# Kernel tuning notes

Hardware: AMD Instinct MI355X
Metric: run time of the kernel (lower is better)

Reference implementation:

```python
import jax, jax.numpy as jnp
import numpy as np

B, L, IN_DIM, D_MODEL, N_LAYERS = 4, 1024, 64, 512, 3
D_INNER, STATE, DT_RANK, K = 1024, 16, 32, 4  # expand=2, dt_rank=d_model//16, conv kernel 4


def setup_inputs() -> dict:
    key = jax.random.key(0)
    ks = jax.random.split(key, 8)
    s = 0.02
    def rn(k, shp):
        return jax.random.normal(k, shp, jnp.float32) * s
    inp = {"x": jax.random.normal(ks[0], (B, L, IN_DIM), jnp.float32)}
    inp["input_w"] = rn(ks[1], (D_MODEL, IN_DIM)); inp["input_b"] = jnp.zeros((D_MODEL,), jnp.float32)
    inp["in_proj_w"] = rn(ks[2], (N_LAYERS, 2 * D_INNER, D_MODEL)); inp["in_proj_b"] = jnp.zeros((N_LAYERS, 2 * D_INNER), jnp.float32)
    inp["conv_w"] = rn(ks[3], (N_LAYERS, D_INNER, 1, K)); inp["conv_b"] = jnp.zeros((N_LAYERS, D_INNER), jnp.float32)
    inp["x_proj_w"] = rn(ks[4], (N_LAYERS, DT_RANK + 2 * STATE, D_INNER))
    inp["dt_proj_w"] = rn(ks[5], (N_LAYERS, D_INNER, DT_RANK)); inp["dt_proj_b"] = jnp.full((N_LAYERS, D_INNER), -4.0, jnp.float32)
    inp["A_log"] = jnp.tile(jnp.log(jnp.arange(1, STATE + 1, dtype=jnp.float32))[None, None, :], (N_LAYERS, D_INNER, 1))
    inp["D"] = jnp.ones((N_LAYERS, D_INNER), jnp.float32)
    inp["out_proj_w"] = rn(ks[6], (N_LAYERS, D_MODEL, D_INNER)); inp["out_proj_b"] = jnp.zeros((N_LAYERS, D_MODEL), jnp.float32)
    inp["ln_w"] = jnp.ones((N_LAYERS, D_MODEL), jnp.float32); inp["ln_b"] = jnp.zeros((N_LAYERS, D_MODEL), jnp.float32)
    return inp


def _layernorm(x, w, b):
    mu = jnp.mean(x, -1, keepdims=True)
    v = jnp.var(x, -1, keepdims=True)
    return (x - mu) * jax.lax.rsqrt(v + 1e-5) * w + b


def _mamba(u, iw, ib, cw, cb, xw, dw, db, A_log, Dp, ow, ob):
    # u: [B, L, d_model]
    xz = u @ iw.T + ib                          # [B, L, 2*d_inner]
    xp, z = jnp.split(xz, 2, axis=-1)
    # causal depthwise conv over time
    xc = jax.lax.conv_general_dilated(xp.transpose(0, 2, 1), cw, (1,), [(K - 1, 0)],
                                      feature_group_count=D_INNER,
                                      dimension_numbers=("NCH", "OIH", "NCH")) + cb[None, :, None]
    xc = jax.nn.silu(xc).transpose(0, 2, 1)     # [B, L, d_inner]
    proj = xc @ xw.T                            # [B, L, dt_rank + 2*N]
    dtl = proj[..., :DT_RANK]
    Bm = proj[..., DT_RANK:DT_RANK + STATE]
    Cm = proj[..., DT_RANK + STATE:]
    dt = jax.nn.softplus(dtl @ dw.T + db)       # [B, L, d_inner]
    A = -jnp.exp(A_log)                         # [d_inner, N]

    def step(h, t):
        dt_t, B_t, C_t, x_t = t                 # [B,d], [B,N], [B,N], [B,d]
        h = h * jnp.exp(dt_t[..., None] * A) + (dt_t * x_t)[..., None] * B_t[:, None, :]
        return h, jnp.einsum("bdn,bn->bd", h, C_t)

    h0 = jnp.zeros((u.shape[0], D_INNER, STATE), u.dtype)
    _, ys = jax.lax.scan(step, h0, (dt.transpose(1, 0, 2), Bm.transpose(1, 0, 2),
                                    Cm.transpose(1, 0, 2), xc.transpose(1, 0, 2)))
    y = ys.transpose(1, 0, 2) + xc * Dp
    y = y * jax.nn.silu(z)
    return y @ ow.T + ob


def reference(x, input_w, input_b, in_proj_w, in_proj_b, conv_w, conv_b, x_proj_w,
              dt_proj_w, dt_proj_b, A_log, D, out_proj_w, out_proj_b, ln_w, ln_b):
    h = x @ input_w.T + input_b                 # [B, L, d_model]
    for i in range(N_LAYERS):
        res = h
        h = _mamba(h, in_proj_w[i], in_proj_b[i], conv_w[i], conv_b[i], x_proj_w[i],
                   dt_proj_w[i], dt_proj_b[i], A_log[i], D[i], out_proj_w[i], out_proj_b[i])
        h = _layernorm(h + res, ln_w[i], ln_b[i])
    return h[:, -1, :]
```

## Files before the change

kernel.cpp:

```cpp
#include <hip/hip_runtime.h>
#include <hip/hip_bf16.h>
#include <cstddef>
#include <cstdint>

#define NB 4
#define NL 1024
#define IN_DIM 64
#define D_MODEL 512
#define N_LAYERS 3
#define D_INNER 1024
#define NSTATE 16
#define DT_RANK 32
#define KCONV 4
#define NROWS (NB * NL)
#define CHUNK 16
#define NCHUNK (NL / CHUNK)
#define LOG2E 1.4426950408889634f

typedef __attribute__((ext_vector_type(8))) short short8;
typedef __attribute__((ext_vector_type(4))) float f32x4;
typedef __attribute__((ext_vector_type(4))) unsigned short us4;
typedef unsigned short ushort_t;

__device__ __forceinline__ ushort_t f2b1(float x) {
  uint32_t u = __builtin_bit_cast(uint32_t, x);
  u += 0x7fffu + ((u >> 16) & 1u);
  return (ushort_t)(u >> 16);
}
__device__ __forceinline__ float b2f(ushort_t u) {
  return __builtin_bit_cast(float, (uint32_t)u << 16);
}

__device__ __forceinline__ void gload_lds16(const ushort_t* src, short* dst) {
  __builtin_amdgcn_global_load_lds(
      (const __attribute__((address_space(1))) uint32_t*)src,
      (__attribute__((address_space(3))) uint32_t*)dst, 16, 0, 0);
}

#define E0 (NROWS * IN_DIM)
#define E1 (D_MODEL * IN_DIM)
#define E2 (N_LAYERS * 2 * D_INNER * D_MODEL)
#define E3 (N_LAYERS * 64 * D_INNER)
#define E4 (N_LAYERS * D_INNER * DT_RANK)
#define E5 (N_LAYERS * D_MODEL * D_INNER)
#define ETOT (E0 + E1 + E2 + E3 + E4 + E5)

__global__ __launch_bounds__(256) void cvt_all(
    const float* __restrict__ x, const float* __restrict__ inw,
    const float* __restrict__ ipw, const float* __restrict__ xpw,
    const float* __restrict__ dpw, const float* __restrict__ opw,
    ushort_t* __restrict__ xb, ushort_t* __restrict__ inwb,
    ushort_t* __restrict__ iwb, ushort_t* __restrict__ xwb,
    ushort_t* __restrict__ dwb, ushort_t* __restrict__ owb)
{
  int i = (blockIdx.x * 256 + threadIdx.x) * 4;
  if (i >= ETOT) return;
  const float* src; ushort_t* dst; int off;
  if      (i < E0)                  { src = x;   dst = xb;   off = i; }
  else if (i < E0+E1)               { src = inw; dst = inwb; off = i - E0; }
  else if (i < E0+E1+E2)            { src = ipw; dst = iwb;  off = i - (E0+E1); }
  else if (i < E0+E1+E2+E3)         { src = xpw; dst = xwb;  off = i - (E0+E1+E2); }
  else if (i < E0+E1+E2+E3+E4)      { src = dpw; dst = dwb;  off = i - (E0+E1+E2+E3); }
  else                              { src = opw; dst = owb;  off = i - (E0+E1+E2+E3+E4); }
  const float4 v = *(const float4*)(src + off);
  us4 o;
  o.x = f2b1(v.x); o.y = f2b1(v.y); o.z = f2b1(v.z); o.w = f2b1(v.w);
  *(us4*)(dst + off) = o;
}

template<int BM, int BN, int MF, int NF, int ACT, bool WF32, bool WB16>
__global__ __launch_bounds__(256) void gemm_mfma(
    const ushort_t* __restrict__ A, int lda,
    const ushort_t* __restrict__ W,
    const float* __restrict__ bias,
    float* __restrict__ Cf, ushort_t* __restrict__ Cb,
    int M, int N, int K)
{
  constexpr int CA = BM / 64;
  constexpr int CB = BN / 64;
  __shared__ __align__(16) short sa[BM * 32];
  __shared__ __align__(16) short sb[BN * 32];

  const int tid = threadIdx.x;
  const int l = tid & 63;
  const int wid = tid >> 6;
  const int wrow = (wid >> 1) * (BM / 2);
  const int wcol = (wid & 1) * (BN / 2);
  const int m0 = blockIdx.y * BM;
  const int n0 = blockIdx.x * BN;

  const int srow = l >> 2;
  const int scol = (l & 3) * 8;

  f32x4 acc[MF][NF] = {};

  for (int k0 = 0; k0 < K; k0 += 32) {
#pragma unroll
    for (int c = 0; c < CA; ++c) {
      short* dst = sa + (c * 4 + wid) * 512;
      const ushort_t* src =
          A + (size_t)(m0 + (c * 4 + wid) * 16 + srow) * lda + k0 + scol;
      gload_lds16(src, dst);
    }
#pragma unroll
    for (int c = 0; c < CB; ++c) {
      short* dst = sb + (c * 4 + wid) * 512;
      const ushort_t* src =
          W + (size_t)(n0 + (c * 4 + wid) * 16 + srow) * K + k0 + scol;
      gload_lds16(src, dst);
    }
    __syncthreads();

    short8 af[MF], bfr[NF];
#pragma unroll
    for (int mi = 0; mi < MF; ++mi)
      af[mi] = *(const short8*)(sa + (wrow + mi * 16 + (l & 15)) * 32 + (l >> 4) * 8);
#pragma unroll
    for (int nj = 0; nj < NF; ++nj)
      bfr[nj] = *(const short8*)(sb + (wcol + nj * 16 + (l & 15)) * 32 + (l >> 4) * 8);
#pragma unroll
    for (int mi = 0; mi < MF; ++mi)
#pragma unroll
      for (int nj = 0; nj < NF; ++nj)
        acc[mi][nj] = __builtin_amdgcn_mfma_f32_16x16x32_bf16(
            af[mi], bfr[nj], acc[mi][nj], 0, 0, 0);
    __syncthreads();
  }

#pragma unroll
  for (int nj = 0; nj < NF; ++nj) {
    const int col = n0 + wcol + nj * 16 + (l & 15);
    const float bv = bias ? bias[col] : 0.f;
#pragma unroll
    for (int mi = 0; mi < MF; ++mi) {
#pragma unroll
      for (int q = 0; q < 4; ++q) {
        const int row = m0 + wrow + mi * 16 + (l >> 4) * 4 + q;
        float v = acc[mi][nj][q] + bv;
        if (ACT == 1) v = (v > 20.f) ? v : log1pf(__expf(v));
        if (WF32) Cf[(size_t)row * N + col] = v;
        if (WB16) Cb[(size_t)row * N + col] = f2b1(v);
      }
    }
  }
}

__global__ __launch_bounds__(256) void conv_silu(
    const ushort_t* __restrict__ xzb,
    const float* __restrict__ cw,
    const float* __restrict__ cb,
    ushort_t* __restrict__ xcb)
{
  const int idx = blockIdx.x * 256 + threadIdx.x;
  const int d4 = (idx & (D_INNER / 4 - 1)) * 4;
  const int bt = idx >> 8;
  const int t = bt & (NL - 1);
  const int b = bt >> 10;

  float acc4[4];
  {
    const float4 cbv = *(const float4*)(cb + d4);
    acc4[0] = cbv.x; acc4[1] = cbv.y; acc4[2] = cbv.z; acc4[3] = cbv.w;
  }
  float wv[4][4];
#pragma unroll
  for (int i = 0; i < 4; ++i) {
    const float4 w = *(const float4*)(cw + (size_t)(d4 + i) * KCONV);
    wv[i][0] = w.x; wv[i][1] = w.y; wv[i][2] = w.z; wv[i][3] = w.w;
  }
#pragma unroll
  for (int j = 0; j < KCONV; ++j) {
    const int tt = t - (KCONV - 1) + j;
    if (tt >= 0) {
      const us4 xv = *(const us4*)(xzb + (size_t)(b * NL + tt) * (2 * D_INNER) + d4);
      acc4[0] = fmaf(b2f(xv.x), wv[0][j], acc4[0]);
      acc4[1] = fmaf(b2f(xv.y), wv[1][j], acc4[1]);
      acc4[2] = fmaf(b2f(xv.z), wv[2][j], acc4[2]);
      acc4[3] = fmaf(b2f(xv.w), wv[3][j], acc4[3]);
    }
  }
  us4 o;
#pragma unroll
  for (int i = 0; i < 4; ++i) {
    const float s = acc4[i] / (1.f + __expf(-acc4[i]));
    ((ushort_t*)&o)[i] = f2b1(s);
  }
  *(us4*)(xcb + (size_t)idx * 4) = o;
}

__global__ __launch_bounds__(256) void scan_fused(
    const ushort_t* __restrict__ dtb,
    const float* __restrict__ proj,
    const ushort_t* __restrict__ xcb,
    const ushort_t* __restrict__ xzb,
    const float* __restrict__ A_log,
    const float* __restrict__ Dp,
    ushort_t* __restrict__ yb)
{
  __shared__ float S_lds[NCHUNK][4][NSTATE + 1];
  __shared__ float H_lds[NCHUNK][4][NSTATE + 1];
  __shared__ float sdt_lds[NCHUNK][4];

  const int tid = threadIdx.x;
  const int c = tid >> 2;
  const int dl = tid & 3;
  const int d = blockIdx.x * 4 + dl;
  const int b = blockIdx.y;

  float A2[NSTATE];
#pragma unroll
  for (int n = 0; n < NSTATE; ++n)
    A2[n] = -__expf(A_log[d * NSTATE + n]) * LOG2E;

  const int t0 = c * CHUNK;
  float h[NSTATE];
#pragma unroll
  for (int n = 0; n < NSTATE; ++n) h[n] = 0.f;
  float sdt = 0.f;

  for (int tt = 0; tt < CHUNK; ++tt) {
    const size_t row = (size_t)(b * NL + t0 + tt);
    const float dtv = b2f(dtb[row * D_INNER + d]);
    const float xv = b2f(xcb[row * D_INNER + d]);
    const float* pr = proj + row * 64;
    float Bv[NSTATE];
    *(float4*)(Bv)      = *(const float4*)(pr + 32);
    *(float4*)(Bv + 4)  = *(const float4*)(pr + 36);
    *(float4*)(Bv + 8)  = *(const float4*)(pr + 40);
    *(float4*)(Bv + 12) = *(const float4*)(pr + 44);
    sdt += dtv;
    const float dx = dtv * xv;
#pragma unroll
    for (int n = 0; n < NSTATE; ++n)
      h[n] = fmaf(h[n], exp2f(dtv * A2[n]), dx * Bv[n]);
  }
  sdt_lds[c][dl] = sdt;
#pragma unroll
  for (int n = 0; n < NSTATE; ++n) S_lds[c][dl][n] = h[n];
  __syncthreads();

  if (tid < 64) {
    const int dl2 = tid >> 4;
    const int n2 = tid & 15;
    const float A2n = -__expf(A_log[(blockIdx.x * 4 + dl2) * NSTATE + n2]) * LOG2E;
    float H = 0.f;
    for (int cc = 0; cc < NCHUNK; ++cc) {
      H_lds[cc][dl2][n2] = H;
      H = fmaf(H, exp2f(A2n * sdt_lds[cc][dl2]), S_lds[cc][dl2][n2]);
    }
  }
  __syncthreads();

#pragma unroll
  for (int n = 0; n < NSTATE; ++n) h[n] = H_lds[c][dl][n];
  const float Dv = Dp[d];

  for (int tt = 0; tt < CHUNK; ++tt) {
    const size_t row = (size_t)(b * NL + t0 + tt);
    const size_t rd = row * D_INNER + d;
    const float dtv = b2f(dtb[rd]);
    const float xv = b2f(xcb[rd]);
    const float* pr = proj + row * 64;
    float Bv[NSTATE], Cv[NSTATE];
    *(float4*)(Bv)      = *(const float4*)(pr + 32);
    *(float4*)(Bv + 4)  = *(const float4*)(pr + 36);
    *(float4*)(Bv + 8)  = *(const float4*)(pr + 40);
    *(float4*)(Bv + 12) = *(const float4*)(pr + 44);
    *(float4*)(Cv)      = *(const float4*)(pr + 48);
    *(float4*)(Cv + 4)  = *(const float4*)(pr + 52);
    *(float4*)(Cv + 8)  = *(const float4*)(pr + 56);
    *(float4*)(Cv + 12) = *(const float4*)(pr + 60);
    const float dx = dtv * xv;
    float accv = 0.f;
#pragma unroll
    for (int n = 0; n < NSTATE; ++n) {
      h[n] = fmaf(h[n], exp2f(dtv * A2[n]), dx * Bv[n]);
      accv = fmaf(h[n], Cv[n], accv);
    }
    const float zv = b2f(xzb[row * (2 * D_INNER) + D_INNER + d]);
    float yv = fmaf(xv, Dv, accv);
    yv *= zv / (1.f + __expf(-zv));
    yb[rd] = f2b1(yv);
  }
}

__global__ __launch_bounds__(256) void add_ln(
    const float* __restrict__ x,
    const float* __restrict__ res,
    const float* __restrict__ w,
    const float* __restrict__ bln,
    float* __restrict__ out,
    ushort_t* __restrict__ outb,
    float* __restrict__ out2)
{
  const int wave = threadIdx.x >> 6;
  const int lane = threadIdx.x & 63;
  const int row = blockIdx.x * 4 + wave;
  const float* xr = x + (size_t)row * D_MODEL;
  const float* rr = res + (size_t)row * D_MODEL;

  float v[8];
  float s = 0.f, s2 = 0.f;
#pragma unroll
  for (int i = 0; i < 8; ++i) {
    const float t = xr[lane + i * 64] + rr[lane + i * 64];
    v[i] = t; s += t; s2 = fmaf(t, t, s2);
  }
#pragma unroll
  for (int off = 32; off; off >>= 1) {
    s += __shfl_xor(s, off);
    s2 += __shfl_xor(s2, off);
  }
  const float mean = s * (1.f / D_MODEL);
  const float var = s2 * (1.f / D_MODEL) - mean * mean;
  const float rstd = rsqrtf(var + 1e-5f);
  const bool last_t = (row & (NL - 1)) == (NL - 1);
#pragma unroll
  for (int i = 0; i < 8; ++i) {
    const int c = lane + i * 64;
    const float o = (v[i] - mean) * rstd * w[c] + bln[c];
    out[(size_t)row * D_MODEL + c] = o;
    outb[(size_t)row * D_MODEL + c] = f2b1(o);
    if (out2 && last_t) out2[(size_t)(row >> 10) * D_MODEL + c] = o;
  }
}

extern "C" void kernel_launch(void* const* d_in, const int* in_sizes, int n_in,
                              void* d_out, int out_size, void* d_ws, size_t ws_size,
                              hipStream_t stream)
{
  const float* x         = (const float*)d_in[0];
  const float* input_w   = (const float*)d_in[1];
  const float* input_b   = (const float*)d_in[2];
  const float* in_proj_w = (const float*)d_in[3];
  const float* in_proj_b = (const float*)d_in[4];
  const float* conv_w    = (const float*)d_in[5];
  const float* conv_b    = (const float*)d_in[6];
  const float* x_proj_w  = (const float*)d_in[7];
  const float* dt_proj_w = (const float*)d_in[8];
  const float* dt_proj_b = (const float*)d_in[9];
  const float* A_log     = (const float*)d_in[10];
  const float* Dp        = (const float*)d_in[11];
  const float* out_proj_w= (const float*)d_in[12];
  const float* out_proj_b= (const float*)d_in[13];
  const float* ln_w      = (const float*)d_in[14];
  const float* ln_b      = (const float*)d_in[15];

  float* p = (float*)d_ws;
  float* h0   = p; p += (size_t)NROWS * D_MODEL;
  float* h1   = p; p += (size_t)NROWS * D_MODEL;
  float* tmp  = p; p += (size_t)NROWS * D_MODEL;
  float* proj = p; p += (size_t)NROWS * 64;
  ushort_t* q = (ushort_t*)p;
  ushort_t* xzb   = q; q += (size_t)NROWS * 2 * D_INNER;
  ushort_t* xcb   = q; q += (size_t)NROWS * D_INNER;
  ushort_t* dtbb  = q; q += (size_t)NROWS * D_INNER;
  ushort_t* projb = q; q += (size_t)NROWS * 64;
  ushort_t* yb    = q; q += (size_t)NROWS * D_INNER;
  ushort_t* hb    = q; q += (size_t)NROWS * D_MODEL;
  ushort_t* xb    = q; q += (size_t)E0;
  ushort_t* inwb  = q; q += (size_t)E1;
  ushort_t* iwb   = q; q += (size_t)E2;
  ushort_t* xwb   = q; q += (size_t)E3;
  ushort_t* dwb   = q; q += (size_t)E4;
  ushort_t* owb   = q; q += (size_t)E5;

  cvt_all<<<(ETOT / 4 + 255) / 256, 256, 0, stream>>>(
      x, input_w, in_proj_w, x_proj_w, dt_proj_w, out_proj_w,
      xb, inwb, iwb, xwb, dwb, owb);

  gemm_mfma<64, 64, 2, 2, 0, true, true>
      <<<dim3(D_MODEL / 64, NROWS / 64), 256, 0, stream>>>(
      xb, IN_DIM, inwb, input_b, h0, hb, NROWS, D_MODEL, IN_DIM);

  float* hc = h0;
  float* hn = h1;

  for (int l = 0; l < N_LAYERS; ++l) {
    const ushort_t* iw = iwb + (size_t)l * 2 * D_INNER * D_MODEL;
    const float* ib = in_proj_b + (size_t)l * 2 * D_INNER;
    const float* cw = conv_w    + (size_t)l * D_INNER * KCONV;
    const float* cb = conv_b    + (size_t)l * D_INNER;
    const ushort_t* xw = xwb + (size_t)l * 64 * D_INNER;
    const ushort_t* dw = dwb + (size_t)l * D_INNER * DT_RANK;
    const float* db = dt_proj_b + (size_t)l * D_INNER;
    const float* Al = A_log     + (size_t)l * D_INNER * NSTATE;
    const float* Dl = Dp        + (size_t)l * D_INNER;
    const ushort_t* ow = owb + (size_t)l * D_MODEL * D_INNER;
    const float* ob = out_proj_b+ (size_t)l * D_MODEL;
    const float* lw = ln_w      + (size_t)l * D_MODEL;
    const float* lb = ln_b      + (size_t)l * D_MODEL;

    gemm_mfma<128, 128, 4, 4, 0, false, true>
        <<<dim3(2 * D_INNER / 128, NROWS / 128), 256, 0, stream>>>(
        hb, D_MODEL, iw, ib, nullptr, xzb, NROWS, 2 * D_INNER, D_MODEL);

    conv_silu<<<NROWS * D_INNER / 4 / 256, 256, 0, stream>>>(xzb, cw, cb, xcb);

    gemm_mfma<64, 64, 2, 2, 0, true, true>
        <<<dim3(1, NROWS / 64), 256, 0, stream>>>(
        xcb, D_INNER, xw, nullptr, proj, projb, NROWS, 64, D_INNER);

    gemm_mfma<128, 128, 4, 4, 1, false, true>
        <<<dim3(D_INNER / 128, NROWS / 128), 256, 0, stream>>>(
        projb, 64, dw, db, nullptr, dtbb, NROWS, D_INNER, DT_RANK);

    scan_fused<<<dim3(D_INNER / 4, NB), 256, 0, stream>>>(
        dtbb, proj, xcb, xzb, Al, Dl, yb);

    gemm_mfma<64, 64, 2, 2, 0, true, false>
        <<<dim3(D_MODEL / 64, NROWS / 64), 256, 0, stream>>>(
        yb, D_INNER, ow, ob, tmp, nullptr, NROWS, D_MODEL, D_INNER);

    add_ln<<<NROWS / 4, 256, 0, stream>>>(
        tmp, hc, lw, lb, hn, hb,
        (l == N_LAYERS - 1) ? (float*)d_out : nullptr);

    float* t2 = hc; hc = hn; hn = t2;
  }
}
```

Measured before the change: 634.8 us.

## Split fused chunked scan into three kernels with coalesced d-major thread mapping

Replaces the single fused chunked-scan kernel, which mapped 4 channels by 64 chunks per block and did the carry through LDS, with three kernels. Phase 1 computes per-chunk local states, a separate carry kernel propagates chunk states across time, and phase 2 recomputes the outputs. Threads now map to consecutive channels, so loads of dt and x are coalesced. The cost is extra global round-trips for the chunk states and two more launches. The out_proj GEMM tile also grows from 64x64 to 128x128, which launches fewer, larger blocks.

```diff
diff --git a/kernel.cpp b/kernel.cpp
--- a/kernel.cpp
+++ b/kernel.cpp
@@ -188,36 +188,30 @@
   *(us4*)(xcb + (size_t)idx * 4) = o;
 }
 
-__global__ __launch_bounds__(256) void scan_fused(
+__global__ __launch_bounds__(256) void scan_phase1(
     const ushort_t* __restrict__ dtb,
     const float* __restrict__ proj,
     const ushort_t* __restrict__ xcb,
-    const ushort_t* __restrict__ xzb,
     const float* __restrict__ A_log,
-    const float* __restrict__ Dp,
-    ushort_t* __restrict__ yb)
-{
-  __shared__ float S_lds[NCHUNK][4][NSTATE + 1];
-  __shared__ float H_lds[NCHUNK][4][NSTATE + 1];
-  __shared__ float sdt_lds[NCHUNK][4];
-
-  const int tid = threadIdx.x;
-  const int c = tid >> 2;
-  const int dl = tid & 3;
-  const int d = blockIdx.x * 4 + dl;
-  const int b = blockIdx.y;
+    float* __restrict__ S_loc,
+    float* __restrict__ sumdt)
+{
+  const int d = blockIdx.x * 256 + threadIdx.x;
+  const int c = blockIdx.y;
+  const int b = blockIdx.z;
 
   float A2[NSTATE];
 #pragma unroll
   for (int n = 0; n < NSTATE; ++n)
     A2[n] = -__expf(A_log[d * NSTATE + n]) * LOG2E;
 
-  const int t0 = c * CHUNK;
   float h[NSTATE];
 #pragma unroll
   for (int n = 0; n < NSTATE; ++n) h[n] = 0.f;
   float sdt = 0.f;
 
+  const int t0 = c * CHUNK;
+#pragma unroll 4
   for (int tt = 0; tt < CHUNK; ++tt) {
     const size_t row = (size_t)(b * NL + t0 + tt);
     const float dtv = b2f(dtb[row * D_INNER + d]);
@@ -234,27 +228,65 @@
     for (int n = 0; n < NSTATE; ++n)
       h[n] = fmaf(h[n], exp2f(dtv * A2[n]), dx * Bv[n]);
   }
-  sdt_lds[c][dl] = sdt;
-#pragma unroll
-  for (int n = 0; n < NSTATE; ++n) S_lds[c][dl][n] = h[n];
-  __syncthreads();
-
-  if (tid < 64) {
-    const int dl2 = tid >> 4;
-    const int n2 = tid & 15;
-    const float A2n = -__expf(A_log[(blockIdx.x * 4 + dl2) * NSTATE + n2]) * LOG2E;
-    float H = 0.f;
-    for (int cc = 0; cc < NCHUNK; ++cc) {
-      H_lds[cc][dl2][n2] = H;
-      H = fmaf(H, exp2f(A2n * sdt_lds[cc][dl2]), S_lds[cc][dl2][n2]);
-    }
-  }
-  __syncthreads();
-
-#pragma unroll
-  for (int n = 0; n < NSTATE; ++n) h[n] = H_lds[c][dl][n];
+
+  const size_t cbase = (size_t)(b * NCHUNK + c);
+  sumdt[cbase * D_INNER + d] = sdt;
+#pragma unroll
+  for (int n = 0; n < NSTATE; ++n)
+    S_loc[(cbase * NSTATE + n) * D_INNER + d] = h[n];
+}
+
+__global__ __launch_bounds__(256) void scan_carry(
+    const float* __restrict__ S_loc,
+    const float* __restrict__ sumdt,
+    const float* __restrict__ A_log,
+    float* __restrict__ H_in)
+{
+  const int idx = blockIdx.x * 256 + threadIdx.x;
+  const int d = idx & (D_INNER - 1);
+  const int n = (idx >> 10) & (NSTATE - 1);
+  const int b = idx >> 14;
+
+  const float A2n = -__expf(A_log[d * NSTATE + n]) * LOG2E;
+
+  float H = 0.f;
+  for (int c = 0; c < NCHUNK; ++c) {
+    const size_t cbase = (size_t)(b * NCHUNK + c);
+    H_in[(cbase * NSTATE + n) * D_INNER + d] = H;
+    const float sdt = sumdt[cbase * D_INNER + d];
+    H = fmaf(H, exp2f(A2n * sdt), S_loc[(cbase * NSTATE + n) * D_INNER + d]);
+  }
+}
+
+__global__ __launch_bounds__(256) void scan_phase2(
+    const ushort_t* __restrict__ dtb,
+    const float* __restrict__ proj,
+    const ushort_t* __restrict__ xcb,
+    const ushort_t* __restrict__ xzb,
+    const float* __restrict__ A_log,
+    const float* __restrict__ Dp,
+    const float* __restrict__ H_in,
+    ushort_t* __restrict__ yb)
+{
+  const int d = blockIdx.x * 256 + threadIdx.x;
+  const int c = blockIdx.y;
+  const int b = blockIdx.z;
+
+  float A2[NSTATE];
+#pragma unroll
+  for (int n = 0; n < NSTATE; ++n)
+    A2[n] = -__expf(A_log[d * NSTATE + n]) * LOG2E;
+
+  const size_t cbase = (size_t)(b * NCHUNK + c);
+  float h[NSTATE];
+#pragma unroll
+  for (int n = 0; n < NSTATE; ++n)
+    h[n] = H_in[(cbase * NSTATE + n) * D_INNER + d];
+
   const float Dv = Dp[d];
-
+  const int t0 = c * CHUNK;
+
+#pragma unroll 4
   for (int tt = 0; tt < CHUNK; ++tt) {
     const size_t row = (size_t)(b * NL + t0 + tt);
     const size_t rd = row * D_INNER + d;
@@ -351,6 +383,9 @@
   float* h1   = p; p += (size_t)NROWS * D_MODEL;
   float* tmp  = p; p += (size_t)NROWS * D_MODEL;
   float* proj = p; p += (size_t)NROWS * 64;
+  float* Sloc = p; p += (size_t)NB * NCHUNK * NSTATE * D_INNER;
+  float* Hin  = p; p += (size_t)NB * NCHUNK * NSTATE * D_INNER;
+  float* sdt  = p; p += (size_t)NB * NCHUNK * D_INNER;
   ushort_t* q = (ushort_t*)p;
   ushort_t* xzb   = q; q += (size_t)NROWS * 2 * D_INNER;
   ushort_t* xcb   = q; q += (size_t)NROWS * D_INNER;
@@ -405,11 +440,15 @@
         <<<dim3(D_INNER / 128, NROWS / 128), 256, 0, stream>>>(
         projb, 64, dw, db, nullptr, dtbb, NROWS, D_INNER, DT_RANK);
 
-    scan_fused<<<dim3(D_INNER / 4, NB), 256, 0, stream>>>(
-        dtbb, proj, xcb, xzb, Al, Dl, yb);
-
-    gemm_mfma<64, 64, 2, 2, 0, true, false>
-        <<<dim3(D_MODEL / 64, NROWS / 64), 256, 0, stream>>>(
+    scan_phase1<<<dim3(D_INNER / 256, NCHUNK, NB), 256, 0, stream>>>(
+        dtbb, proj, xcb, Al, Sloc, sdt);
+    scan_carry<<<(NB * NSTATE * D_INNER) / 256, 256, 0, stream>>>(
+        Sloc, sdt, Al, Hin);
+    scan_phase2<<<dim3(D_INNER / 256, NCHUNK, NB), 256, 0, stream>>>(
+        dtbb, proj, xcb, xzb, Al, Dl, Hin, yb);
+
+    gemm_mfma<128, 128, 4, 4, 0, true, false>
+        <<<dim3(D_MODEL / 128, NROWS / 128), 256, 0, stream>>>(
         yb, D_INNER, ow, ob, tmp, nullptr, NROWS, D_MODEL, D_INNER);
 
     add_ln<<<NROWS / 4, 256, 0, stream>>>(
```

Measured after the change: 599.4 us. -5.6%, faster.
